# Kernel optimization log

Hardware: AMD Instinct MI355X
Metric: run time of the kernel (lower is better)

The kernel has to match this reference:

```python
import jax, jax.numpy as jnp
import numpy as np

EMB, HEADS = 1024, 16
HS = EMB // HEADS
LN_EPS = 1e-5


def _layernorm(v, g, b):
    # normalize over last dim (headsize)
    mu = jnp.mean(v, axis=-1, keepdims=True)
    var = jnp.mean(jnp.square(v - mu), axis=-1, keepdims=True)
    return (v - mu) * jax.lax.rsqrt(var + LN_EPS) * g + b


def setup_inputs() -> dict:
    key = jax.random.key(0)
    ks = jax.random.split(key, 12)
    s = 1.0 / np.sqrt(EMB)
    return {
        "x": jax.random.normal(ks[0], (4, 2048, EMB), dtype=jnp.float32),
        "mask": jax.random.randint(ks[1], (4, 2048), 0, 2, dtype=jnp.int32),
        "Wk": jax.random.uniform(ks[2], (EMB, EMB), jnp.float32, -s, s),
        "Wq": jax.random.uniform(ks[3], (EMB, EMB), jnp.float32, -s, s),
        "Wv": jax.random.uniform(ks[4], (EMB, EMB), jnp.float32, -s, s),
        "Wo": jax.random.uniform(ks[5], (EMB, EMB), jnp.float32, -s, s),
        "bo": jax.random.uniform(ks[6], (EMB,), jnp.float32, -s, s),
        "kln_g": jnp.ones((HS,), jnp.float32),
        "kln_b": jnp.zeros((HS,), jnp.float32),
        "qln_g": jnp.ones((HS,), jnp.float32),
        "qln_b": jnp.zeros((HS,), jnp.float32),
    }


def reference(x, mask, Wk, Wq, Wv, Wo, bo, kln_g, kln_b, qln_g, qln_b):
    b, t, e = x.shape
    # QKV projections (torch Linear: y = x @ W.T), split into heads
    k = (x @ Wk.T).reshape(b, t, HEADS, HS)
    q = (x @ Wq.T).reshape(b, t, HEADS, HS)
    v = (x @ Wv.T).reshape(b, t, HEADS, HS)
    # per-head LayerNorm on K and Q
    k = _layernorm(k, kln_g, kln_b)
    q = _layernorm(q, qln_g, qln_b)
    # scale by emb^(1/4) on each side
    scale = jnp.asarray(e, x.dtype) ** 0.25
    q = q / scale
    k = k / scale
    # [b, h, tq, tk] attention logits
    dot = jnp.einsum("bqhd,bkhd->bhqk", q, k)
    # outer-product mask, broadcast over heads
    m = mask.astype(x.dtype)
    dm = m[:, None, :, None] * m[:, None, None, :]  # [b,1,tq,tk]
    # non-memory-efficient masked softmax: softmax(v*m)*m renormalized
    attn = jax.nn.softmax(dot * dm, axis=-1) * dm
    attn = attn / (jnp.sum(attn, axis=-1, keepdims=True) + 1e-13)
    out = jnp.einsum("bhqk,bkhd->bqhd", attn, v).reshape(b, t, e)
    return out @ Wo.T + bo
```

## Files before the change

kernel.cpp:

```cpp
#include <hip/hip_runtime.h>
#include <math.h>

#define B_SZ   4
#define T_SEQ  2048
#define EMB    1024
#define HEADS  16
#define HS     64
#define M_TOT  (B_SZ * T_SEQ)

typedef unsigned short u16;
using f32x4  = __attribute__((ext_vector_type(4))) float;
using bf16x8 = __attribute__((ext_vector_type(8))) short;
using u16x8  = __attribute__((ext_vector_type(8))) unsigned short;
using u16x4  = __attribute__((ext_vector_type(4))) unsigned short;

__device__ __forceinline__ void async16(u16* lds, const u16* g) {
    __builtin_amdgcn_global_load_lds(
        (const __attribute__((address_space(1))) unsigned int*)g,
        (__attribute__((address_space(3))) unsigned int*)lds, 16, 0, 0);
}

__device__ __forceinline__ u16 bf16_rne(float f) {
    unsigned u = __float_as_uint(f);
    return (u16)((u + 0x7fffu + ((u >> 16) & 1u)) >> 16);
}
__device__ __forceinline__ void split2(float f, u16& h, u16& l) {
    h = bf16_rne(f);
    float hf = __uint_as_float(((unsigned)h) << 16);
    l = bf16_rne(f - hf);
}
__device__ __forceinline__ unsigned cvt_pk_bf16(float a, float b) {
    unsigned r;
    asm("v_cvt_pk_bf16_f32 %0, %1, %2" : "=v"(r) : "v"(a), "v"(b));
    return r;
}

__global__ __launch_bounds__(256) void split_all(
    const float* __restrict__ x,  const float* __restrict__ wq,
    const float* __restrict__ wk, const float* __restrict__ wv,
    const float* __restrict__ wo,
    u16* __restrict__ xh,  u16* __restrict__ xl,
    u16* __restrict__ wqh, u16* __restrict__ wql,
    u16* __restrict__ wkh, u16* __restrict__ wkl,
    u16* __restrict__ wvh, u16* __restrict__ wvl,
    u16* __restrict__ woh, u16* __restrict__ wol)
{
    int i = blockIdx.x * 256 + threadIdx.x;
    int r = i >> 18;
    const float* src; u16* dh; u16* dl; int off;
    if (r < 8)       { src = x;  dh = xh;  dl = xl;  off = i; }
    else if (r == 8) { src = wq; dh = wqh; dl = wql; off = i - (8 << 18); }
    else if (r == 9) { src = wk; dh = wkh; dl = wkl; off = i - (9 << 18); }
    else if (r == 10){ src = wv; dh = wvh; dl = wvl; off = i - (10 << 18); }
    else             { src = wo; dh = woh; dl = wol; off = i - (11 << 18); }
    float4 v = ((const float4*)src)[off];
    float f[4] = {v.x, v.y, v.z, v.w};
    u16 hh[4], ll[4];
    #pragma unroll
    for (int j = 0; j < 4; ++j) split2(f[j], hh[j], ll[j]);
    uint2 H, L;
    H.x = (unsigned)hh[0] | ((unsigned)hh[1] << 16);
    H.y = (unsigned)hh[2] | ((unsigned)hh[3] << 16);
    L.x = (unsigned)ll[0] | ((unsigned)ll[1] << 16);
    L.y = (unsigned)ll[2] | ((unsigned)ll[3] << 16);
    ((uint2*)dh)[off] = H;
    ((uint2*)dl)[off] = L;
}

#define BM 128
#define BN 128
#define BKB 32

__global__ __launch_bounds__(256, 2) void gemm_mfma(
    const u16* __restrict__ Ah, const u16* __restrict__ Al,
    const u16* __restrict__ Wh, const u16* __restrict__ Wl,
    float* __restrict__ Cf, u16* __restrict__ Chi, u16* __restrict__ Clo,
    const float* __restrict__ lng, const float* __restrict__ lnb,
    float post_scale, const float* __restrict__ bias, int mode)
{
    __shared__ u16 sAh[BM * BKB], sAl[BM * BKB];
    __shared__ u16 sBh[BN * BKB], sBl[BN * BKB];
    const int tid = threadIdx.x;
    const int w = tid >> 6, lane = tid & 63;
    const int wr = w >> 1, wc = w & 1;
    const int m0 = blockIdx.x * BM, n0 = blockIdx.y * BN;
    const int fr = lane & 15, kc = (lane >> 4) * 8;
    const int srow = lane >> 2, schunk = (lane & 3) * 8;

    f32x4 acc[4][4] = {};

    for (int k0 = 0; k0 < EMB; k0 += BKB) {
        #pragma unroll
        for (int c = 0; c < 2; ++c) {
            int r = (w * 2 + c) * 16 + srow;
            size_t gA = (size_t)(m0 + r) * EMB + k0 + schunk;
            size_t gB = (size_t)(n0 + r) * EMB + k0 + schunk;
            int lb = (w * 2 + c) * 512;
            async16(&sAh[lb], Ah + gA);
            async16(&sAl[lb], Al + gA);
            async16(&sBh[lb], Wh + gB);
            async16(&sBl[lb], Wl + gB);
        }
        __syncthreads();

        bf16x8 bh[4], bl[4];
        #pragma unroll
        for (int ni = 0; ni < 4; ++ni) {
            int row = wc * 64 + ni * 16 + fr;
            bh[ni] = *(const bf16x8*)&sBh[row * BKB + kc];
            bl[ni] = *(const bf16x8*)&sBl[row * BKB + kc];
        }
        #pragma unroll
        for (int mi = 0; mi < 4; ++mi) {
            int row = wr * 64 + mi * 16 + fr;
            bf16x8 ah = *(const bf16x8*)&sAh[row * BKB + kc];
            bf16x8 al = *(const bf16x8*)&sAl[row * BKB + kc];
            #pragma unroll
            for (int ni = 0; ni < 4; ++ni) {
                acc[mi][ni] = __builtin_amdgcn_mfma_f32_16x16x32_bf16(ah, bh[ni], acc[mi][ni], 0, 0, 0);
                acc[mi][ni] = __builtin_amdgcn_mfma_f32_16x16x32_bf16(ah, bl[ni], acc[mi][ni], 0, 0, 0);
                acc[mi][ni] = __builtin_amdgcn_mfma_f32_16x16x32_bf16(al, bh[ni], acc[mi][ni], 0, 0, 0);
            }
        }
        __syncthreads();
    }

    if (mode == 1) {
        float g4[4], b4[4];
        #pragma unroll
        for (int ni = 0; ni < 4; ++ni) {
            int dd = ni * 16 + fr;
            g4[ni] = lng[dd];
            b4[ni] = lnb[dd];
        }
        #pragma unroll
        for (int mi = 0; mi < 4; ++mi) {
            #pragma unroll
            for (int i = 0; i < 4; ++i) {
                float s = acc[mi][0][i] + acc[mi][1][i] + acc[mi][2][i] + acc[mi][3][i];
                #pragma unroll
                for (int off = 1; off < 16; off <<= 1) s += __shfl_xor(s, off);
                float mu = s * (1.f / HS);
                float d2 = 0.f;
                #pragma unroll
                for (int ni = 0; ni < 4; ++ni) {
                    float d = acc[mi][ni][i] - mu;
                    d2 += d * d;
                }
                #pragma unroll
                for (int off = 1; off < 16; off <<= 1) d2 += __shfl_xor(d2, off);
                float rs = rsqrtf(d2 * (1.f / HS) + 1e-5f);
                #pragma unroll
                for (int ni = 0; ni < 4; ++ni)
                    acc[mi][ni][i] = ((acc[mi][ni][i] - mu) * rs * g4[ni] + b4[ni]) * post_scale;
            }
        }
    }

    #pragma unroll
    for (int mi = 0; mi < 4; ++mi) {
        #pragma unroll
        for (int ni = 0; ni < 4; ++ni) {
            const int col = n0 + wc * 64 + ni * 16 + fr;
            const int rowb = m0 + wr * 64 + mi * 16 + (lane >> 4) * 4;
            if (mode == 0) {
                float badd = bias[col];
                #pragma unroll
                for (int i = 0; i < 4; ++i)
                    Cf[(size_t)(rowb + i) * EMB + col] = acc[mi][ni][i] + badd;
            } else if (mode == 1) {
                #pragma unroll
                for (int i = 0; i < 4; ++i) {
                    u16 hh, ll; split2(acc[mi][ni][i], hh, ll);
                    Chi[(size_t)(rowb + i) * EMB + col] = hh;
                    Clo[(size_t)(rowb + i) * EMB + col] = ll;
                }
            } else {
                int hh = col >> 6, d = col & 63;
                int bb = rowb >> 11, t0 = rowb & 2047;
                u16x4 H, L;
                #pragma unroll
                for (int i = 0; i < 4; ++i) {
                    u16 vh, vl; split2(acc[mi][ni][i], vh, vl);
                    H[i] = vh; L[i] = vl;
                }
                size_t off = ((size_t)((bb * HEADS + hh) * HS + d)) * T_SEQ + t0;
                *(u16x4*)(Chi + off) = H;
                *(u16x4*)(Clo + off) = L;
            }
        }
    }
}

__global__ __launch_bounds__(512, 2) void attn_mfma(
    const u16* __restrict__ qh, const u16* __restrict__ ql,
    const u16* __restrict__ kh, const u16* __restrict__ kl,
    const u16* __restrict__ vh, const u16* __restrict__ vl,
    const int* __restrict__ mask,
    u16* __restrict__ oh, u16* __restrict__ ol)
{
    __shared__ u16 sKh[64 * 72], sKl[64 * 72], sVh[64 * 72], sVl[64 * 72];
    __shared__ u16 sPs[8][32 * 72];
    __shared__ float kmsh[64];
    __shared__ float qmsh[256];
    __shared__ float fb[8][32];

    const int tid = threadIdx.x;
    const int w = tid >> 6, lane = tid & 63;
    const int fr = lane & 15, g = lane >> 4;
    const int q0 = blockIdx.x * 256;
    const int h = blockIdx.y, b = blockIdx.z;

    if (tid < 256) qmsh[tid] = (float)mask[b * T_SEQ + q0 + tid];

    const int bsel = w >> 1, half = w & 1;
    const u16* gsrc; u16* sdst; int rstr; size_t kstep;
    if (bsel == 0)      { gsrc = kh + (size_t)b * T_SEQ * EMB + h * HS; sdst = sKh; rstr = EMB;   kstep = (size_t)64 * EMB; }
    else if (bsel == 1) { gsrc = kl + (size_t)b * T_SEQ * EMB + h * HS; sdst = sKl; rstr = EMB;   kstep = (size_t)64 * EMB; }
    else if (bsel == 2) { gsrc = vh + (size_t)(b * HEADS + h) * HS * T_SEQ; sdst = sVh; rstr = T_SEQ; kstep = 64; }
    else                { gsrc = vl + (size_t)(b * HEADS + h) * HS * T_SEQ; sdst = sVl; rstr = T_SEQ; kstep = 64; }
    gsrc += (size_t)half * 32 * rstr;
    sdst += half * 32 * 72;

    bf16x8 qfh[2][2], qfl[2][2];
    #pragma unroll
    for (int nf = 0; nf < 2; ++nf)
        #pragma unroll
        for (int ks = 0; ks < 2; ++ks) {
            size_t off = (size_t)(b * T_SEQ + q0 + w * 32 + nf * 16 + fr) * EMB
                         + h * HS + g * 8 + ks * 32;
            qfh[nf][ks] = *(const bf16x8*)(qh + off);
            qfl[nf][ks] = *(const bf16x8*)(ql + off);
        }

    f32x4 o[2][4] = {};
    float mrun[2] = {-INFINITY, -INFINITY}, lrun[2] = {0.f, 0.f};
    u16* Psw = sPs[w];

    for (int kt = 0; kt < T_SEQ / 64; ++kt) {
        const u16* src = gsrc + (size_t)kt * kstep;
        u16x8 stg[4];
        #pragma unroll
        for (int it = 0; it < 4; ++it) {
            int idx = it * 64 + lane;
            stg[it] = *(const u16x8*)(src + (size_t)(idx >> 3) * rstr + (idx & 7) * 8);
        }
        #pragma unroll
        for (int it = 0; it < 4; ++it) {
            int idx = it * 64 + lane;
            *(u16x8*)&sdst[(idx >> 3) * 72 + (idx & 7) * 8] = stg[it];
        }
        if (tid < 64) kmsh[tid] = (float)mask[b * T_SEQ + kt * 64 + tid];
        __syncthreads();

        float kmv[4][4]; int anyv = 0;
        #pragma unroll
        for (int mf = 0; mf < 4; ++mf)
            #pragma unroll
            for (int i = 0; i < 4; ++i) {
                kmv[mf][i] = kmsh[mf * 16 + g * 4 + i];
                anyv |= (kmv[mf][i] != 0.f);
            }

        if (__any(anyv)) {
            f32x4 st[4][2] = {};
            #pragma unroll
            for (int ks = 0; ks < 2; ++ks) {
                bf16x8 ka[4], kb[4];
                #pragma unroll
                for (int mf = 0; mf < 4; ++mf) {
                    ka[mf] = *(const bf16x8*)&sKh[(mf * 16 + fr) * 72 + g * 8 + ks * 32];
                    kb[mf] = *(const bf16x8*)&sKl[(mf * 16 + fr) * 72 + g * 8 + ks * 32];
                }
                __builtin_amdgcn_s_setprio(1);
                #pragma unroll
                for (int mf = 0; mf < 4; ++mf)
                    #pragma unroll
                    for (int nf = 0; nf < 2; ++nf) {
                        st[mf][nf] = __builtin_amdgcn_mfma_f32_16x16x32_bf16(ka[mf], qfh[nf][ks], st[mf][nf], 0, 0, 0);
                        st[mf][nf] = __builtin_amdgcn_mfma_f32_16x16x32_bf16(ka[mf], qfl[nf][ks], st[mf][nf], 0, 0, 0);
                        st[mf][nf] = __builtin_amdgcn_mfma_f32_16x16x32_bf16(kb[mf], qfh[nf][ks], st[mf][nf], 0, 0, 0);
                    }
                __builtin_amdgcn_s_setprio(0);
            }
            #pragma unroll
            for (int nf = 0; nf < 2; ++nf) {
                float tm = -INFINITY;
                #pragma unroll
                for (int mf = 0; mf < 4; ++mf)
                    #pragma unroll
                    for (int i = 0; i < 4; ++i) {
                        float s = (kmv[mf][i] != 0.f) ? st[mf][nf][i] : -INFINITY;
                        st[mf][nf][i] = s;
                        tm = fmaxf(tm, s);
                    }
                tm = fmaxf(tm, __shfl_xor(tm, 16));
                tm = fmaxf(tm, __shfl_xor(tm, 32));
                float mn = fmaxf(mrun[nf], tm);
                if (mn != -INFINITY) {
                    float f = __expf(mrun[nf] - mn);
                    float ps = 0.f;
                    #pragma unroll
                    for (int mf = 0; mf < 4; ++mf)
                        #pragma unroll
                        for (int i = 0; i < 4; ++i) {
                            float p = __expf(st[mf][nf][i] - mn);
                            st[mf][nf][i] = p;
                            ps += p;
                        }
                    ps += __shfl_xor(ps, 16);
                    ps += __shfl_xor(ps, 32);
                    lrun[nf] = lrun[nf] * f + ps;
                    mrun[nf] = mn;
                    fb[w][nf * 16 + fr] = f;
                } else {
                    #pragma unroll
                    for (int mf = 0; mf < 4; ++mf)
                        #pragma unroll
                        for (int i = 0; i < 4; ++i) st[mf][nf][i] = 0.f;
                    fb[w][nf * 16 + fr] = 1.f;
                }
            }
            #pragma unroll
            for (int nf = 0; nf < 2; ++nf)
                #pragma unroll
                for (int mf = 0; mf < 4; ++mf)
                    #pragma unroll
                    for (int i = 0; i < 4; i += 2) {
                        unsigned pk = cvt_pk_bf16(st[mf][nf][i], st[mf][nf][i + 1]);
                        *(unsigned*)&Psw[(nf * 16 + fr) * 72 + mf * 16 + g * 4 + i] = pk;
                    }
            float ff[2][4];
            #pragma unroll
            for (int mi = 0; mi < 2; ++mi)
                #pragma unroll
                for (int i = 0; i < 4; ++i)
                    ff[mi][i] = fb[w][mi * 16 + g * 4 + i];
            #pragma unroll
            for (int mi = 0; mi < 2; ++mi)
                #pragma unroll
                for (int nj = 0; nj < 4; ++nj)
                    #pragma unroll
                    for (int i = 0; i < 4; ++i)
                        o[mi][nj][i] *= ff[mi][i];
            #pragma unroll
            for (int ks = 0; ks < 2; ++ks) {
                bf16x8 pa[2];
                #pragma unroll
                for (int mi = 0; mi < 2; ++mi)
                    pa[mi] = *(const bf16x8*)&Psw[(mi * 16 + fr) * 72 + g * 8 + ks * 32];
                __builtin_amdgcn_s_setprio(1);
                #pragma unroll
                for (int nj = 0; nj < 4; ++nj) {
                    bf16x8 va = *(const bf16x8*)&sVh[(nj * 16 + fr) * 72 + g * 8 + ks * 32];
                    bf16x8 vb = *(const bf16x8*)&sVl[(nj * 16 + fr) * 72 + g * 8 + ks * 32];
                    #pragma unroll
                    for (int mi = 0; mi < 2; ++mi) {
                        o[mi][nj] = __builtin_amdgcn_mfma_f32_16x16x32_bf16(pa[mi], va, o[mi][nj], 0, 0, 0);
                        o[mi][nj] = __builtin_amdgcn_mfma_f32_16x16x32_bf16(pa[mi], vb, o[mi][nj], 0, 0, 0);
                    }
                }
                __builtin_amdgcn_s_setprio(0);
            }
        }
        __syncthreads();
    }

    #pragma unroll
    for (int nf = 0; nf < 2; ++nf) fb[w][nf * 16 + fr] = lrun[nf];
    #pragma unroll
    for (int mi = 0; mi < 2; ++mi) {
        #pragma unroll
        for (int i = 0; i < 4; ++i) {
            float lq = fb[w][mi * 16 + g * 4 + i];
            float qv = qmsh[w * 32 + mi * 16 + g * 4 + i];
            float inv = (qv != 0.f && lq > 0.f) ? 1.f / lq : 0.f;
            size_t row = (size_t)(b * T_SEQ + q0 + w * 32 + mi * 16 + g * 4 + i);
            #pragma unroll
            for (int nj = 0; nj < 4; ++nj) {
                float v = o[mi][nj][i] * inv;
                u16 hh, ll; split2(v, hh, ll);
                size_t off = row * EMB + h * HS + nj * 16 + fr;
                oh[off] = hh;
                ol[off] = ll;
            }
        }
    }
}

extern "C" void kernel_launch(void* const* d_in, const int* in_sizes, int n_in,
                              void* d_out, int out_size, void* d_ws, size_t ws_size,
                              hipStream_t stream)
{
    const float* x    = (const float*)d_in[0];
    const int*   mask = (const int*)d_in[1];
    const float* Wk   = (const float*)d_in[2];
    const float* Wq   = (const float*)d_in[3];
    const float* Wv   = (const float*)d_in[4];
    const float* Wo   = (const float*)d_in[5];
    const float* bo   = (const float*)d_in[6];
    const float* kg   = (const float*)d_in[7];
    const float* kbb  = (const float*)d_in[8];
    const float* qg   = (const float*)d_in[9];
    const float* qbb  = (const float*)d_in[10];
    float* out = (float*)d_out;

    const size_t NELT = (size_t)M_TOT * EMB;
    const size_t WELT = (size_t)EMB * EMB;
    u16* xh  = (u16*)d_ws;
    u16* xl  = xh + NELT;
    u16* p_qh = xl + NELT;
    u16* p_ql = p_qh + NELT;
    u16* p_kh = p_ql + NELT;
    u16* p_kl = p_kh + NELT;
    u16* p_vh = p_kl + NELT;
    u16* p_vl = p_vh + NELT;
    u16* wqh = p_vl + NELT;
    u16* wql = wqh + WELT;
    u16* wkh = wql + WELT;
    u16* wkl = wkh + WELT;
    u16* wvh = wkl + WELT;
    u16* wvl = wvh + WELT;
    u16* woh = wvl + WELT;
    u16* wol = woh + WELT;

    const float ps = 0.17677669529663687f;

    split_all<<<12288, 256, 0, stream>>>(x, Wq, Wk, Wv, Wo,
        xh, xl, wqh, wql, wkh, wkl, wvh, wvl, woh, wol);

    dim3 ggrid(M_TOT / BM, EMB / BN);
    gemm_mfma<<<ggrid, 256, 0, stream>>>(xh, xl, wqh, wql, nullptr, p_qh, p_ql, qg, qbb, ps, nullptr, 1);
    gemm_mfma<<<ggrid, 256, 0, stream>>>(xh, xl, wkh, wkl, nullptr, p_kh, p_kl, kg, kbb, ps, nullptr, 1);
    gemm_mfma<<<ggrid, 256, 0, stream>>>(xh, xl, wvh, wvl, nullptr, p_vh, p_vl, nullptr, nullptr, 1.f, nullptr, 2);

    dim3 agrid(T_SEQ / 256, HEADS, B_SZ);
    attn_mfma<<<agrid, 512, 0, stream>>>(p_qh, p_ql, p_kh, p_kl, p_vh, p_vl, mask, xh, xl);

    gemm_mfma<<<ggrid, 256, 0, stream>>>(xh, xl, woh, wol, out, nullptr, nullptr, nullptr, nullptr, 1.f, bo, 0);
}
```

Baseline: 568.1 us.

## Prefetch next K/V tile, swizzle LDS, use exp2 with lazy softmax rescale

Global loads for the next K/V tile and the mask chunk are issued into registers right after the barrier, so they overlap with the current tile's MFMA work. The padded 72-stride LDS rows become unpadded 64-stride rows with an XOR chunk swizzle, which cuts LDS footprint while aiming to avoid bank conflicts. The softmax now uses exp2, with log2(e) folded into the Q projection scale, and rescales the output accumulator only when the running max grows by more than a threshold (FA4-style lazy rescale). This trades extra register pressure from the staging buffers for less latency and fewer exp/rescale operations, with some numerical risk from the deferred-max threshold.

```diff
diff --git a/kernel.cpp b/kernel.cpp
--- a/kernel.cpp
+++ b/kernel.cpp
@@ -13,6 +13,8 @@
 using bf16x8 = __attribute__((ext_vector_type(8))) short;
 using u16x8  = __attribute__((ext_vector_type(8))) unsigned short;
 using u16x4  = __attribute__((ext_vector_type(4))) unsigned short;
+
+#define EXP2F(x) __builtin_amdgcn_exp2f(x)
 
 __device__ __forceinline__ void async16(u16* lds, const u16* g) {
     __builtin_amdgcn_global_load_lds(
@@ -199,8 +201,8 @@
     const int* __restrict__ mask,
     u16* __restrict__ oh, u16* __restrict__ ol)
 {
-    __shared__ u16 sKh[64 * 72], sKl[64 * 72], sVh[64 * 72], sVl[64 * 72];
-    __shared__ u16 sPs[8][32 * 72];
+    __shared__ u16 sKh[64 * 64], sKl[64 * 64], sVh[64 * 64], sVl[64 * 64];
+    __shared__ u16 sPs[8][32 * 64];
     __shared__ float kmsh[64];
     __shared__ float qmsh[256];
     __shared__ float fb[8][32];
@@ -208,6 +210,7 @@
     const int tid = threadIdx.x;
     const int w = tid >> 6, lane = tid & 63;
     const int fr = lane & 15, g = lane >> 4;
+    const int xr = fr & 7;
     const int q0 = blockIdx.x * 256;
     const int h = blockIdx.y, b = blockIdx.z;
 
@@ -220,7 +223,11 @@
     else if (bsel == 2) { gsrc = vh + (size_t)(b * HEADS + h) * HS * T_SEQ; sdst = sVh; rstr = T_SEQ; kstep = 64; }
     else                { gsrc = vl + (size_t)(b * HEADS + h) * HS * T_SEQ; sdst = sVl; rstr = T_SEQ; kstep = 64; }
     gsrc += (size_t)half * 32 * rstr;
-    sdst += half * 32 * 72;
+    sdst += half * 32 * 64;
+    const int wrow = lane >> 3;
+    const int wchunk = (lane & 7) ^ wrow;
+    const u16* lsrc = gsrc + (size_t)wrow * rstr + (lane & 7) * 8;
+    u16* ldst = sdst + wrow * 64 + (wchunk << 3);
 
     bf16x8 qfh[2][2], qfl[2][2];
     #pragma unroll
@@ -237,21 +244,27 @@
     float mrun[2] = {-INFINITY, -INFINITY}, lrun[2] = {0.f, 0.f};
     u16* Psw = sPs[w];
 
-    for (int kt = 0; kt < T_SEQ / 64; ++kt) {
-        const u16* src = gsrc + (size_t)kt * kstep;
-        u16x8 stg[4];
-        #pragma unroll
-        for (int it = 0; it < 4; ++it) {
-            int idx = it * 64 + lane;
-            stg[it] = *(const u16x8*)(src + (size_t)(idx >> 3) * rstr + (idx & 7) * 8);
-        }
-        #pragma unroll
-        for (int it = 0; it < 4; ++it) {
-            int idx = it * 64 + lane;
-            *(u16x8*)&sdst[(idx >> 3) * 72 + (idx & 7) * 8] = stg[it];
-        }
-        if (tid < 64) kmsh[tid] = (float)mask[b * T_SEQ + kt * 64 + tid];
+    u16x8 stg[4];
+    #pragma unroll
+    for (int it = 0; it < 4; ++it)
+        stg[it] = *(const u16x8*)(lsrc + (size_t)it * 8 * rstr);
+    int kmreg = mask[b * T_SEQ + (tid & 63)];
+
+    const int NT = T_SEQ / 64;
+    for (int kt = 0; kt < NT; ++kt) {
+        #pragma unroll
+        for (int it = 0; it < 4; ++it)
+            *(u16x8*)(ldst + it * 8 * 64) = stg[it];
+        if (tid < 64) kmsh[tid] = (float)kmreg;
         __syncthreads();
+
+        if (kt + 1 < NT) {
+            const u16* s = lsrc + (size_t)(kt + 1) * kstep;
+            #pragma unroll
+            for (int it = 0; it < 4; ++it)
+                stg[it] = *(const u16x8*)(s + (size_t)it * 8 * rstr);
+            kmreg = mask[b * T_SEQ + (kt + 1) * 64 + (tid & 63)];
+        }
 
         float kmv[4][4]; int anyv = 0;
         #pragma unroll
@@ -269,8 +282,9 @@
                 bf16x8 ka[4], kb[4];
                 #pragma unroll
                 for (int mf = 0; mf < 4; ++mf) {
-                    ka[mf] = *(const bf16x8*)&sKh[(mf * 16 + fr) * 72 + g * 8 + ks * 32];
-                    kb[mf] = *(const bf16x8*)&sKl[(mf * 16 + fr) * 72 + g * 8 + ks * 32];
+                    int ridx = ((mf * 16 + fr) << 6) + (((g + 4 * ks) ^ xr) << 3);
+                    ka[mf] = *(const bf16x8*)&sKh[ridx];
+                    kb[mf] = *(const bf16x8*)&sKl[ridx];
                 }
                 __builtin_amdgcn_s_setprio(1);
                 #pragma unroll
@@ -296,64 +310,61 @@
                     }
                 tm = fmaxf(tm, __shfl_xor(tm, 16));
                 tm = fmaxf(tm, __shfl_xor(tm, 32));
-                float mn = fmaxf(mrun[nf], tm);
-                if (mn != -INFINITY) {
-                    float f = __expf(mrun[nf] - mn);
-                    float ps = 0.f;
-                    #pragma unroll
-                    for (int mf = 0; mf < 4; ++mf)
-                        #pragma unroll
-                        for (int i = 0; i < 4; ++i) {
-                            float p = __expf(st[mf][nf][i] - mn);
-                            st[mf][nf][i] = p;
-                            ps += p;
-                        }
-                    ps += __shfl_xor(ps, 16);
-                    ps += __shfl_xor(ps, 32);
-                    lrun[nf] = lrun[nf] * f + ps;
+                if (!__all(tm <= mrun[nf] + 8.0f)) {
+                    float mn = fmaxf(mrun[nf], tm);
+                    float f = EXP2F(mrun[nf] - mn);
+                    fb[w][nf * 16 + fr] = f;
+                    lrun[nf] *= f;
                     mrun[nf] = mn;
-                    fb[w][nf * 16 + fr] = f;
+                    float f0 = fb[w][nf * 16 + g * 4 + 0];
+                    float f1 = fb[w][nf * 16 + g * 4 + 1];
+                    float f2 = fb[w][nf * 16 + g * 4 + 2];
+                    float f3 = fb[w][nf * 16 + g * 4 + 3];
+                    #pragma unroll
+                    for (int nj = 0; nj < 4; ++nj) {
+                        o[nf][nj][0] *= f0; o[nf][nj][1] *= f1;
+                        o[nf][nj][2] *= f2; o[nf][nj][3] *= f3;
+                    }
+                }
+                if (mrun[nf] > -1e37f) {
+                    float ps_ = 0.f;
+                    #pragma unroll
+                    for (int mf = 0; mf < 4; ++mf) {
+                        float p0 = EXP2F(st[mf][nf][0] - mrun[nf]);
+                        float p1 = EXP2F(st[mf][nf][1] - mrun[nf]);
+                        float p2 = EXP2F(st[mf][nf][2] - mrun[nf]);
+                        float p3 = EXP2F(st[mf][nf][3] - mrun[nf]);
+                        ps_ += (p0 + p1) + (p2 + p3);
+                        int idx = ((nf * 16 + fr) << 6)
+                                + (((2 * mf + (g >> 1)) ^ xr) << 3) + (g & 1) * 4;
+                        *(unsigned*)&Psw[idx]     = cvt_pk_bf16(p0, p1);
+                        *(unsigned*)&Psw[idx + 2] = cvt_pk_bf16(p2, p3);
+                    }
+                    ps_ += __shfl_xor(ps_, 16);
+                    ps_ += __shfl_xor(ps_, 32);
+                    lrun[nf] += ps_;
                 } else {
                     #pragma unroll
-                    for (int mf = 0; mf < 4; ++mf)
-                        #pragma unroll
-                        for (int i = 0; i < 4; ++i) st[mf][nf][i] = 0.f;
-                    fb[w][nf * 16 + fr] = 1.f;
-                }
-            }
-            #pragma unroll
-            for (int nf = 0; nf < 2; ++nf)
-                #pragma unroll
-                for (int mf = 0; mf < 4; ++mf)
-                    #pragma unroll
-                    for (int i = 0; i < 4; i += 2) {
-                        unsigned pk = cvt_pk_bf16(st[mf][nf][i], st[mf][nf][i + 1]);
-                        *(unsigned*)&Psw[(nf * 16 + fr) * 72 + mf * 16 + g * 4 + i] = pk;
-                    }
-            float ff[2][4];
-            #pragma unroll
-            for (int mi = 0; mi < 2; ++mi)
-                #pragma unroll
-                for (int i = 0; i < 4; ++i)
-                    ff[mi][i] = fb[w][mi * 16 + g * 4 + i];
-            #pragma unroll
-            for (int mi = 0; mi < 2; ++mi)
-                #pragma unroll
-                for (int nj = 0; nj < 4; ++nj)
-                    #pragma unroll
-                    for (int i = 0; i < 4; ++i)
-                        o[mi][nj][i] *= ff[mi][i];
+                    for (int mf = 0; mf < 4; ++mf) {
+                        int idx = ((nf * 16 + fr) << 6)
+                                + (((2 * mf + (g >> 1)) ^ xr) << 3) + (g & 1) * 4;
+                        *(unsigned*)&Psw[idx]     = 0u;
+                        *(unsigned*)&Psw[idx + 2] = 0u;
+                    }
+                }
+            }
             #pragma unroll
             for (int ks = 0; ks < 2; ++ks) {
                 bf16x8 pa[2];
                 #pragma unroll
                 for (int mi = 0; mi < 2; ++mi)
-                    pa[mi] = *(const bf16x8*)&Psw[(mi * 16 + fr) * 72 + g * 8 + ks * 32];
+                    pa[mi] = *(const bf16x8*)&Psw[((mi * 16 + fr) << 6) + (((g + 4 * ks) ^ xr) << 3)];
                 __builtin_amdgcn_s_setprio(1);
                 #pragma unroll
                 for (int nj = 0; nj < 4; ++nj) {
-                    bf16x8 va = *(const bf16x8*)&sVh[(nj * 16 + fr) * 72 + g * 8 + ks * 32];
-                    bf16x8 vb = *(const bf16x8*)&sVl[(nj * 16 + fr) * 72 + g * 8 + ks * 32];
+                    int ridx = ((nj * 16 + fr) << 6) + (((g + 4 * ks) ^ xr) << 3);
+                    bf16x8 va = *(const bf16x8*)&sVh[ridx];
+                    bf16x8 vb = *(const bf16x8*)&sVl[ridx];
                     #pragma unroll
                     for (int mi = 0; mi < 2; ++mi) {
                         o[mi][nj] = __builtin_amdgcn_mfma_f32_16x16x32_bf16(pa[mi], va, o[mi][nj], 0, 0, 0);
@@ -424,13 +435,14 @@
     u16* woh = wvl + WELT;
     u16* wol = woh + WELT;
 
-    const float ps = 0.17677669529663687f;
+    const float ps   = 0.17677669529663687f;
+    const float ps_q = 0.17677669529663687f * 1.44269504088896f;
 
     split_all<<<12288, 256, 0, stream>>>(x, Wq, Wk, Wv, Wo,
         xh, xl, wqh, wql, wkh, wkl, wvh, wvl, woh, wol);
 
     dim3 ggrid(M_TOT / BM, EMB / BN);
-    gemm_mfma<<<ggrid, 256, 0, stream>>>(xh, xl, wqh, wql, nullptr, p_qh, p_ql, qg, qbb, ps, nullptr, 1);
+    gemm_mfma<<<ggrid, 256, 0, stream>>>(xh, xl, wqh, wql, nullptr, p_qh, p_ql, qg, qbb, ps_q, nullptr, 1);
     gemm_mfma<<<ggrid, 256, 0, stream>>>(xh, xl, wkh, wkl, nullptr, p_kh, p_kl, kg, kbb, ps, nullptr, 1);
     gemm_mfma<<<ggrid, 256, 0, stream>>>(xh, xl, wvh, wvl, nullptr, p_vh, p_vl, nullptr, nullptr, 1.f, nullptr, 2);
 
```

Result: faster. 515.9 us (-9.2%).
